# Kernel optimization log

Measured on AMD Instinct MI355X. Metric: run time of the kernel, lower is better.

## Reference

```python
import jax, jax.numpy as jnp
import numpy as np
import math

GROUPS = 32
EPS = 1e-5

def group_norm(x, w, b):
    B, C, H, W = x.shape
    xg = x.reshape(B, GROUPS, C // GROUPS, H, W)
    mu = xg.mean(axis=(2, 3, 4), keepdims=True)
    var = xg.var(axis=(2, 3, 4), keepdims=True)
    xn = ((xg - mu) * jax.lax.rsqrt(var + EPS)).reshape(B, C, H, W)
    return xn * w[None, :, None, None] + b[None, :, None, None]

def conv1x1(x, w, b):
    # x: [B,Cin,H,W], w: [Cout,Cin], b: [Cout]
    return jnp.einsum('bchw,oc->bohw', x, w) + b[None, :, None, None]

def setup_inputs() -> dict:
    key = jax.random.key(0)
    ks = jax.random.split(key, 8)
    B, C, E, H, W = 8, 256, 512, 64, 64
    x = jax.random.normal(ks[0], (B, C, H, W), dtype=jnp.float32)
    condA = jax.random.normal(ks[1], (B, E, H, W), dtype=jnp.float32)
    gn_x_w = jnp.ones((C,), jnp.float32)
    gn_x_b = jnp.zeros((C,), jnp.float32)
    gn_c_w = jnp.ones((E,), jnp.float32)
    gn_c_b = jnp.zeros((E,), jnp.float32)
    q_w = jax.random.normal(ks[2], (C, C), jnp.float32) * 0.02
    q_b = jnp.zeros((C,), jnp.float32)
    k_w = jax.random.normal(ks[3], (C, E), jnp.float32) * 0.02
    k_b = jnp.zeros((C,), jnp.float32)
    v_w = jax.random.normal(ks[4], (C, E), jnp.float32) * 0.02
    v_b = jnp.zeros((C,), jnp.float32)
    return {"x": x, "condA": condA, "gn_x_w": gn_x_w, "gn_x_b": gn_x_b,
            "gn_c_w": gn_c_w, "gn_c_b": gn_c_b, "q_w": q_w, "q_b": q_b,
            "k_w": k_w, "k_b": k_b, "v_w": v_w, "v_b": v_b}

def reference(x, condA, gn_x_w, gn_x_b, gn_c_w, gn_c_b, q_w, q_b, k_w, k_b, v_w, v_b):
    B, C, H, W = x.shape
    scale = math.sqrt(C)
    h = group_norm(x, gn_x_w, gn_x_b)
    h1 = group_norm(condA, gn_c_w, gn_c_b)
    q = conv1x1(h, q_w, q_b)      # [B,C,H,W]
    k = conv1x1(h1, k_w, k_b)     # [B,C,Hc,Wc]
    v = conv1x1(h1, v_w, v_b)     # [B,C,Hc,Wc]
    qf = q.transpose(0, 2, 3, 1).reshape(B, H * W, C)        # [B,N,C]
    kf = k.reshape(B, C, -1)                                  # [B,C,M]
    vf = v.transpose(0, 2, 3, 1).reshape(B, -1, C)            # [B,M,C]
    attn = jax.nn.softmax(jnp.einsum('bnc,bcm->bnm', qf, kf) / scale, axis=-1)
    out = jnp.einsum('bnm,bmc->bnc', attn, vf)                # [B,N,C]
    return out.reshape(B, H, W, C).transpose(0, 3, 1, 2)
```

## Files before the change

### kernel.cpp

```cpp
#include <hip/hip_runtime.h>


typedef _Float16 half8 __attribute__((ext_vector_type(8)));
typedef _Float16 half4v __attribute__((ext_vector_type(4)));
typedef float f32x4 __attribute__((ext_vector_type(4)));
typedef float f32x16 __attribute__((ext_vector_type(16)));

#define MFMA16(a, b, c) __builtin_amdgcn_mfma_f32_16x16x32_f16((a), (b), (c), 0, 0, 0)
#define MFMA32(a, b, c) __builtin_amdgcn_mfma_f32_32x32x16_f16((a), (b), (c), 0, 0, 0)

__global__ __launch_bounds__(256) void stats_kernel(
    const float* __restrict__ x, const float* __restrict__ condA,
    float* __restrict__ sx, float* __restrict__ sc) {
  int id = blockIdx.x;
  const float4* src;
  int nf4;
  float* dst;
  float inv_n;
  if (id < 256) {
    src = (const float4*)(x + (size_t)id * 32768);
    nf4 = 8192;
    dst = sx + id * 2;
    inv_n = 1.0f / 32768.0f;
  } else {
    int j = id - 256;
    src = (const float4*)(condA + (size_t)j * 65536);
    nf4 = 16384;
    dst = sc + j * 2;
    inv_n = 1.0f / 65536.0f;
  }
  int t = threadIdx.x;
  float s = 0.f, s2 = 0.f;
  for (int i = t; i < nf4; i += 256) {
    float4 v = src[i];
    s += v.x + v.y + v.z + v.w;
    s2 += v.x * v.x + v.y * v.y + v.z * v.z + v.w * v.w;
  }
#pragma unroll
  for (int m = 1; m <= 32; m <<= 1) {
    s += __shfl_xor(s, m, 64);
    s2 += __shfl_xor(s2, m, 64);
  }
  __shared__ float red[8];
  int w = t >> 6;
  if ((t & 63) == 0) { red[w * 2] = s; red[w * 2 + 1] = s2; }
  __syncthreads();
  if (t == 0) {
    float S = red[0] + red[2] + red[4] + red[6];
    float S2 = red[1] + red[3] + red[5] + red[7];
    float mu = S * inv_n;
    float var = S2 * inv_n - mu * mu;
    dst[0] = mu;
    dst[1] = rsqrtf(var + 1e-5f);
  }
}

template <int CH, int GS>
__global__ __launch_bounds__(256) void ntrans_kernel(
    const float* __restrict__ src, const float* __restrict__ stats,
    const float* __restrict__ gw, const float* __restrict__ gb,
    _Float16* __restrict__ dst) {
  int bid = blockIdx.x;
  int b = bid & 7, nt = (bid >> 3) & 63, ctile = bid >> 9;
  int n0 = nt * 64, c0 = ctile * 64;
  int t = threadIdx.x;
  __shared__ float tile[64][65];

  int cl = t >> 2;
  int c = c0 + cl;
  const float* st = stats + ((size_t)b * 32 + (c / GS)) * 2;
  float mu = st[0], rs = st[1];
  float a = rs * gw[c];
  float bb = gb[c] - mu * a;
  const float* srow = src + ((size_t)(b * CH + c)) * 4096 + n0 + (t & 3) * 16;
#pragma unroll
  for (int i = 0; i < 4; i++) {
    float4 v = *(const float4*)(srow + 4 * i);
    int nn = (t & 3) * 16 + 4 * i;
    tile[cl][nn + 0] = v.x * a + bb;
    tile[cl][nn + 1] = v.y * a + bb;
    tile[cl][nn + 2] = v.z * a + bb;
    tile[cl][nn + 3] = v.w * a + bb;
  }
  __syncthreads();
  int nl = t >> 2;
  half8 ov[2];
#pragma unroll
  for (int u = 0; u < 2; u++)
#pragma unroll
    for (int i = 0; i < 8; i++) ov[u][i] = (_Float16)tile[(t & 3) * 16 + 8 * u + i][nl];
  int n = n0 + nl;
  size_t tb = ((size_t)b * 256 + (n >> 4)) * (CH / 32);
  int ca = c0 + (t & 3) * 16;
#pragma unroll
  for (int u = 0; u < 2; u++) {
    int cc = ca + 8 * u;
    size_t addr = ((tb + (cc >> 5)) * 64 + (n & 15) + 16 * ((cc >> 3) & 3)) * 8;
    *(half8*)(dst + addr) = ov[u];
  }
}

__global__ __launch_bounds__(256) void wconv_kernel(
    const float* __restrict__ wq, const float* __restrict__ wk,
    const float* __restrict__ wv, _Float16* __restrict__ wqt,
    _Float16* __restrict__ wkt, _Float16* __restrict__ wvt) {
  int i = blockIdx.x * 256 + threadIdx.x;
  const float* src;
  _Float16* dst;
  int cin, ksbits, gi;
  if (i < 8192) { src = wq; dst = wqt; cin = 256; ksbits = 3; gi = i; }
  else if (i < 24576) { src = wk; dst = wkt; cin = 512; ksbits = 4; gi = i - 8192; }
  else if (i < 40960) { src = wv; dst = wvt; cin = 512; ksbits = 4; gi = i - 24576; }
  else return;
  int tile = gi >> 6, g = gi & 63;
  int otile = tile >> ksbits, ks = tile & ((1 << ksbits) - 1);
  int o = otile * 16 + (g & 15), k = ks * 32 + (g >> 4) * 8;
  const float* s = src + (size_t)o * cin + k;
  half8 hv;
#pragma unroll
  for (int j = 0; j < 8; j++) hv[j] = (_Float16)s[j];
  *(half8*)(dst + (size_t)gi * 8) = hv;
}

template <int CIN, int SCALE>
__global__ __launch_bounds__(256, 2) void projQK_kernel(
    const _Float16* __restrict__ Ht, const _Float16* __restrict__ Wt,
    const float* __restrict__ bias, _Float16* __restrict__ out) {
  int bid = blockIdx.x;
  int b = bid & 7, nt = (bid >> 3) & 31, ot = bid >> 8;
  int n0 = nt * 128, o0 = ot * 64;
  int t = threadIdx.x, l = t & 63, w = t >> 6;
  int c15 = l & 15, q = l >> 4;
  constexpr int KS = CIN / 32;

  const half8* ap = (const half8*)Wt + ((size_t)(ot * 4 + w) * KS) * 64 + l;
  const half8* bp = (const half8*)Ht + ((size_t)(b * 256 + nt * 8) * KS) * 64 + l;

  f32x4 acc[8] = {};
#pragma unroll
  for (int ks = 0; ks < KS; ks++) {
    half8 af = ap[ks * 64];
#pragma unroll
    for (int ct = 0; ct < 8; ct++)
      acc[ct] = MFMA16(af, bp[(ct * KS + ks) * 64], acc[ct]);
  }
  int o4 = o0 + w * 16 + 4 * q;
  f32x4 bv = *(const f32x4*)(bias + o4);
#pragma unroll
  for (int ct = 0; ct < 8; ct++) {
    int n = n0 + ct * 16 + c15;
    half4v hv;
#pragma unroll
    for (int r = 0; r < 4; r++) {
      float v = acc[ct][r] + bv[r];
      if (SCALE) v *= 0.0625f;
      hv[r] = (_Float16)v;
    }
    *(half4v*)(out + ((size_t)b * 4096 + n) * 256 + o4) = hv;
  }
}

__global__ __launch_bounds__(256, 2) void projV_kernel(
    const _Float16* __restrict__ Ht, const _Float16* __restrict__ Wt,
    const float* __restrict__ bias, _Float16* __restrict__ Vt) {
  int bid = blockIdx.x;
  int b = bid & 7, mt = (bid >> 3) & 63, ct2 = bid >> 9;
  int m0 = mt * 64, c0 = ct2 * 128;
  int t = threadIdx.x, l = t & 63, w = t >> 6;
  int c15 = l & 15, q = l >> 4;
  constexpr int KS = 16;

  const half8* ap = (const half8*)Ht + ((size_t)(b * 256 + mt * 4 + w) * KS) * 64 + l;
  const half8* bp = (const half8*)Wt + ((size_t)(c0 >> 4) * KS) * 64 + l;

  f32x4 acc[8] = {};
#pragma unroll
  for (int ks = 0; ks < KS; ks++) {
    half8 af = ap[ks * 64];
#pragma unroll
    for (int ct = 0; ct < 8; ct++)
      acc[ct] = MFMA16(af, bp[(ct * KS + ks) * 64], acc[ct]);
  }
  int m = m0 + w * 16 + 4 * q;
  size_t mbase = ((size_t)b * 256 + (m >> 4)) * 8;
#pragma unroll
  for (int ct = 0; ct < 8; ct++) {
    int c = c0 + ct * 16 + c15;
    float bs = bias[c];
    half4v pv4;
#pragma unroll
    for (int r = 0; r < 4; r++) pv4[r] = (_Float16)(acc[ct][r] + bs);
    size_t addr = ((mbase + (c >> 5)) * 64 + (c & 31) + ((q >> 1) << 5)) * 8 + (q & 1) * 4;
    *(half4v*)(Vt + addr) = pv4;
  }
}

__global__ __launch_bounds__(256, 2) void attn_kernel(
    const _Float16* __restrict__ Q, const _Float16* __restrict__ K,
    const _Float16* __restrict__ Vt, float* __restrict__ out) {
  int bid = blockIdx.x;
  int b = bid & 7, nt = bid >> 3;
  int n0 = nt * 64;
  int t = threadIdx.x, l = t & 63, w = t >> 6;
  int l31 = l & 31, h = l >> 5;
  int mh = w & 1, nh = w >> 1;

  __shared__ __align__(16) _Float16 kbuf[16384];
  __shared__ __align__(16) _Float16 pbuf[4096];
  __shared__ float lsw[2][64];

  half8 qf[16];
  {
    const _Float16* qb = Q + ((size_t)(b * 4096 + n0 + nh * 32 + l31)) * 256 + h * 8;
#pragma unroll
    for (int ks = 0; ks < 16; ks++) qf[ks] = *(const half8*)(qb + ks * 16);
  }

  const half8* kgl = (const half8*)(K + ((size_t)b * 4096 + w * 16 + h) * 256) + l31;
  int kwa[8];
  {
    int kblk = l31 >> 1, hw = l & 1;
    int swz = (kblk & 3) << 1;
    int mblk = w >> 1;
#pragma unroll
    for (int i = 0; i < 8; i++) {
      int m5 = ((w & 1) << 4) + 2 * i + h;
      int g = ((m5 ^ hw) | (hw << 5)) ^ swz;
      kwa[i] = (mblk * 16 + kblk) * 512 + g * 8;
    }
  }
  int gbase = (l31 ^ h) | (h << 5);

  const half8* vt8 = (const half8*)Vt + (size_t)b * 256 * 8 * 64;

  f32x16 acc_o[4] = {};
  float l_part = 0.f;

  half8 kreg[8];
#pragma unroll
  for (int i = 0; i < 8; i++) kreg[i] = kgl[i * 64];
#pragma unroll
  for (int i = 0; i < 8; i++) *(half8*)&kbuf[kwa[i]] = kreg[i];
  __syncthreads();

  for (int it = 0; it < 64; it++) {
    int itn = it < 63 ? it + 1 : 63;
#pragma unroll
    for (int i = 0; i < 8; i++) kreg[i] = kgl[itn * 2048 + i * 64];
    half8 vf0[8];
#pragma unroll
    for (int u = 0; u < 2; u++)
#pragma unroll
      for (int ct = 0; ct < 4; ct++)
        vf0[u * 4 + ct] = vt8[((size_t)(it * 4 + u) * 8 + (mh * 4 + ct)) * 64 + l];

    f32x16 s = {};
#pragma unroll
    for (int ks = 0; ks < 16; ks++) {
      half8 kf = *(const half8*)&kbuf[(mh * 16 + ks) * 512 + (gbase ^ ((ks & 3) << 1)) * 8];
      s = MFMA32(kf, qf[ks], s);
    }

    half4v pv[4];
#pragma unroll
    for (int k2 = 0; k2 < 4; k2++) {
#pragma unroll
      for (int r = 0; r < 4; r++) {
        float e = __expf(s[4 * k2 + r]);
        l_part += e;
        pv[k2][r] = (_Float16)e;
      }
    }
    __syncthreads();

#pragma unroll
    for (int k2 = 0; k2 < 4; k2++) {
      int hm = k2 & 1;
      int tau = nh * 4 + mh * 2 + (k2 >> 1);
      int g = (l31 ^ hm) | (hm << 5);
      *(half4v*)&pbuf[tau * 512 + g * 8 + 4 * h] = pv[k2];
    }
#pragma unroll
    for (int i = 0; i < 8; i++) *(half8*)&kbuf[kwa[i]] = kreg[i];
    __syncthreads();

    half8 vf1[8];
#pragma unroll
    for (int u = 0; u < 2; u++)
#pragma unroll
      for (int ct = 0; ct < 4; ct++)
        vf1[u * 4 + ct] = vt8[((size_t)(it * 4 + 2 + u) * 8 + (mh * 4 + ct)) * 64 + l];
#pragma unroll
    for (int ks = 0; ks < 2; ks++) {
      half8 pf = *(const half8*)&pbuf[(nh * 4 + ks) * 512 + gbase * 8];
#pragma unroll
      for (int ct = 0; ct < 4; ct++) acc_o[ct] = MFMA32(pf, vf0[ks * 4 + ct], acc_o[ct]);
    }
#pragma unroll
    for (int ks = 2; ks < 4; ks++) {
      half8 pf = *(const half8*)&pbuf[(nh * 4 + ks) * 512 + gbase * 8];
#pragma unroll
      for (int ct = 0; ct < 4; ct++) acc_o[ct] = MFMA32(pf, vf1[(ks - 2) * 4 + ct], acc_o[ct]);
    }
  }

  {
    float v = l_part + __shfl_xor(l_part, 32, 64);
    if (l < 32) lsw[mh][nh * 32 + l] = v;
  }
  __syncthreads();
#pragma unroll
  for (int k2 = 0; k2 < 4; k2++) {
    int nb = nh * 32 + 4 * h + 8 * k2;
    f32x4 s0 = *(const f32x4*)&lsw[0][nb];
    f32x4 s1 = *(const f32x4*)&lsw[1][nb];
    f32x4 linv;
#pragma unroll
    for (int r = 0; r < 4; r++) linv[r] = 1.0f / (s0[r] + s1[r]);
#pragma unroll
    for (int ct = 0; ct < 4; ct++) {
      int c = mh * 128 + ct * 32 + l31;
      f32x4 o4;
#pragma unroll
      for (int r = 0; r < 4; r++) o4[r] = acc_o[ct][4 * k2 + r] * linv[r];
      *(f32x4*)(out + ((size_t)(b * 256 + c)) * 4096 + n0 + nb) = o4;
    }
  }
}

extern "C" void kernel_launch(void* const* d_in, const int* in_sizes, int n_in,
                              void* d_out, int out_size, void* d_ws,
                              size_t ws_size, hipStream_t stream) {
  const float* x = (const float*)d_in[0];
  const float* condA = (const float*)d_in[1];
  const float* gxw = (const float*)d_in[2];
  const float* gxb = (const float*)d_in[3];
  const float* gcw = (const float*)d_in[4];
  const float* gcb = (const float*)d_in[5];
  const float* qw = (const float*)d_in[6];
  const float* qb = (const float*)d_in[7];
  const float* kw = (const float*)d_in[8];
  const float* kb = (const float*)d_in[9];
  const float* vw = (const float*)d_in[10];
  const float* vb = (const float*)d_in[11];
  float* out = (float*)d_out;

  char* ws = (char*)d_ws;
  float* statsx = (float*)(ws);
  float* statsc = (float*)(ws + 2048);
  _Float16* wqt = (_Float16*)(ws + 4096);
  _Float16* wkt = (_Float16*)(ws + 135168);
  _Float16* wvt = (_Float16*)(ws + 397312);
  char* p = ws + 659456;
  _Float16* hxTt = (_Float16*)p; p += (size_t)8 * 4096 * 256 * 2;
  _Float16* h1Tt = (_Float16*)p; p += (size_t)8 * 4096 * 512 * 2;
  _Float16* Qh = (_Float16*)p;   p += (size_t)8 * 4096 * 256 * 2;
  _Float16* Kh = (_Float16*)p;   p += (size_t)8 * 4096 * 256 * 2;
  _Float16* Vt = (_Float16*)p;

  stats_kernel<<<512, 256, 0, stream>>>(x, condA, statsx, statsc);
  ntrans_kernel<256, 8><<<2048, 256, 0, stream>>>(x, statsx, gxw, gxb, hxTt);
  ntrans_kernel<512, 16><<<4096, 256, 0, stream>>>(condA, statsc, gcw, gcb, h1Tt);
  wconv_kernel<<<160, 256, 0, stream>>>(qw, kw, vw, wqt, wkt, wvt);
  projQK_kernel<256, 1><<<1024, 256, 0, stream>>>(hxTt, wqt, qb, Qh);
  projQK_kernel<512, 0><<<1024, 256, 0, stream>>>(h1Tt, wkt, kb, Kh);
  projV_kernel<<<1024, 256, 0, stream>>>(h1Tt, wvt, vb, Vt);
  attn_kernel<<<512, 256, 0, stream>>>(Qh, Kh, Vt, out);
}
```

Baseline: 441.2 us.

## Merge prep kernels, fuse K/V projections with shared LDS tile, pre-tile Q/K for attention

```diff
diff --git a/kernel.cpp b/kernel.cpp
--- a/kernel.cpp
+++ b/kernel.cpp
@@ -9,27 +9,48 @@
 #define MFMA16(a, b, c) __builtin_amdgcn_mfma_f32_16x16x32_f16((a), (b), (c), 0, 0, 0)
 #define MFMA32(a, b, c) __builtin_amdgcn_mfma_f32_32x32x16_f16((a), (b), (c), 0, 0, 0)
 
-__global__ __launch_bounds__(256) void stats_kernel(
+__global__ __launch_bounds__(256) void statswconv_kernel(
     const float* __restrict__ x, const float* __restrict__ condA,
-    float* __restrict__ sx, float* __restrict__ sc) {
-  int id = blockIdx.x;
+    float* __restrict__ sx, float* __restrict__ sc,
+    const float* __restrict__ wq, const float* __restrict__ wk,
+    const float* __restrict__ wv, _Float16* __restrict__ wqt,
+    _Float16* __restrict__ wkt, _Float16* __restrict__ wvt) {
+  int bid = blockIdx.x;
+  int t = threadIdx.x;
+  if (bid >= 512) {
+    int i = (bid - 512) * 256 + t;
+    const float* src;
+    _Float16* dst;
+    int cin, ksbits, gi;
+    if (i < 8192) { src = wq; dst = wqt; cin = 256; ksbits = 3; gi = i; }
+    else if (i < 24576) { src = wk; dst = wkt; cin = 512; ksbits = 4; gi = i - 8192; }
+    else { src = wv; dst = wvt; cin = 512; ksbits = 4; gi = i - 24576; }
+    int tile = gi >> 6, g = gi & 63;
+    int otile = tile >> ksbits, ks = tile & ((1 << ksbits) - 1);
+    int o = otile * 16 + (g & 15), k = ks * 32 + (g >> 4) * 8;
+    const float* s = src + (size_t)o * cin + k;
+    half8 hv;
+#pragma unroll
+    for (int j = 0; j < 8; j++) hv[j] = (_Float16)s[j];
+    *(half8*)(dst + (size_t)gi * 8) = hv;
+    return;
+  }
   const float4* src;
   int nf4;
   float* dst;
   float inv_n;
-  if (id < 256) {
-    src = (const float4*)(x + (size_t)id * 32768);
+  if (bid < 256) {
+    src = (const float4*)(x + (size_t)bid * 32768);
     nf4 = 8192;
-    dst = sx + id * 2;
+    dst = sx + bid * 2;
     inv_n = 1.0f / 32768.0f;
   } else {
-    int j = id - 256;
+    int j = bid - 256;
     src = (const float4*)(condA + (size_t)j * 65536);
     nf4 = 16384;
     dst = sc + j * 2;
     inv_n = 1.0f / 65536.0f;
   }
-  int t = threadIdx.x;
   float s = 0.f, s2 = 0.f;
   for (int i = t; i < nf4; i += 256) {
     float4 v = src[i];
@@ -55,20 +76,31 @@
   }
 }
 
-template <int CH, int GS>
 __global__ __launch_bounds__(256) void ntrans_kernel(
-    const float* __restrict__ src, const float* __restrict__ stats,
-    const float* __restrict__ gw, const float* __restrict__ gb,
-    _Float16* __restrict__ dst) {
+    const float* __restrict__ x, const float* __restrict__ condA,
+    const float* __restrict__ statsx, const float* __restrict__ statsc,
+    const float* __restrict__ gxw, const float* __restrict__ gxb,
+    const float* __restrict__ gcw, const float* __restrict__ gcb,
+    _Float16* __restrict__ hxTt, _Float16* __restrict__ h1Tt) {
   int bid = blockIdx.x;
-  int b = bid & 7, nt = (bid >> 3) & 63, ctile = bid >> 9;
+  const float *src, *stats, *gw, *gb;
+  _Float16* dst;
+  int CH, gsh, bid2;
+  if (bid < 2048) {
+    src = x; stats = statsx; gw = gxw; gb = gxb; dst = hxTt;
+    CH = 256; gsh = 3; bid2 = bid;
+  } else {
+    src = condA; stats = statsc; gw = gcw; gb = gcb; dst = h1Tt;
+    CH = 512; gsh = 4; bid2 = bid - 2048;
+  }
+  int b = bid2 & 7, nt = (bid2 >> 3) & 63, ctile = bid2 >> 9;
   int n0 = nt * 64, c0 = ctile * 64;
   int t = threadIdx.x;
   __shared__ float tile[64][65];
 
   int cl = t >> 2;
   int c = c0 + cl;
-  const float* st = stats + ((size_t)b * 32 + (c / GS)) * 2;
+  const float* st = stats + ((size_t)b * 32 + (c >> gsh)) * 2;
   float mu = st[0], rs = st[1];
   float a = rs * gw[c];
   float bb = gb[c] - mu * a;
@@ -90,7 +122,7 @@
 #pragma unroll
     for (int i = 0; i < 8; i++) ov[u][i] = (_Float16)tile[(t & 3) * 16 + 8 * u + i][nl];
   int n = n0 + nl;
-  size_t tb = ((size_t)b * 256 + (n >> 4)) * (CH / 32);
+  size_t tb = ((size_t)b * 256 + (n >> 4)) * (CH >> 5);
   int ca = c0 + (t & 3) * 16;
 #pragma unroll
   for (int u = 0; u < 2; u++) {
@@ -100,103 +132,132 @@
   }
 }
 
-__global__ __launch_bounds__(256) void wconv_kernel(
-    const float* __restrict__ wq, const float* __restrict__ wk,
-    const float* __restrict__ wv, _Float16* __restrict__ wqt,
-    _Float16* __restrict__ wkt, _Float16* __restrict__ wvt) {
-  int i = blockIdx.x * 256 + threadIdx.x;
-  const float* src;
-  _Float16* dst;
-  int cin, ksbits, gi;
-  if (i < 8192) { src = wq; dst = wqt; cin = 256; ksbits = 3; gi = i; }
-  else if (i < 24576) { src = wk; dst = wkt; cin = 512; ksbits = 4; gi = i - 8192; }
-  else if (i < 40960) { src = wv; dst = wvt; cin = 512; ksbits = 4; gi = i - 24576; }
-  else return;
-  int tile = gi >> 6, g = gi & 63;
-  int otile = tile >> ksbits, ks = tile & ((1 << ksbits) - 1);
-  int o = otile * 16 + (g & 15), k = ks * 32 + (g >> 4) * 8;
-  const float* s = src + (size_t)o * cin + k;
-  half8 hv;
-#pragma unroll
-  for (int j = 0; j < 8; j++) hv[j] = (_Float16)s[j];
-  *(half8*)(dst + (size_t)gi * 8) = hv;
-}
-
-template <int CIN, int SCALE>
-__global__ __launch_bounds__(256, 2) void projQK_kernel(
+__global__ __launch_bounds__(256, 2) void projQ_kernel(
     const _Float16* __restrict__ Ht, const _Float16* __restrict__ Wt,
-    const float* __restrict__ bias, _Float16* __restrict__ out) {
+    const float* __restrict__ bias, _Float16* __restrict__ Qt) {
   int bid = blockIdx.x;
-  int b = bid & 7, nt = (bid >> 3) & 31, ot = bid >> 8;
-  int n0 = nt * 128, o0 = ot * 64;
+  int b = bid & 7, nt = bid >> 3;
   int t = threadIdx.x, l = t & 63, w = t >> 6;
   int c15 = l & 15, q = l >> 4;
-  constexpr int KS = CIN / 32;
-
-  const half8* ap = (const half8*)Wt + ((size_t)(ot * 4 + w) * KS) * 64 + l;
-  const half8* bp = (const half8*)Ht + ((size_t)(b * 256 + nt * 8) * KS) * 64 + l;
-
-  f32x4 acc[8] = {};
-#pragma unroll
-  for (int ks = 0; ks < KS; ks++) {
-    half8 af = ap[ks * 64];
-#pragma unroll
-    for (int ct = 0; ct < 8; ct++)
-      acc[ct] = MFMA16(af, bp[(ct * KS + ks) * 64], acc[ct]);
-  }
-  int o4 = o0 + w * 16 + 4 * q;
-  f32x4 bv = *(const f32x4*)(bias + o4);
-#pragma unroll
-  for (int ct = 0; ct < 8; ct++) {
-    int n = n0 + ct * 16 + c15;
-    half4v hv;
-#pragma unroll
-    for (int r = 0; r < 4; r++) {
-      float v = acc[ct][r] + bv[r];
-      if (SCALE) v *= 0.0625f;
-      hv[r] = (_Float16)v;
-    }
-    *(half4v*)(out + ((size_t)b * 4096 + n) * 256 + o4) = hv;
-  }
-}
-
-__global__ __launch_bounds__(256, 2) void projV_kernel(
-    const _Float16* __restrict__ Ht, const _Float16* __restrict__ Wt,
-    const float* __restrict__ bias, _Float16* __restrict__ Vt) {
+
+  __shared__ __align__(16) _Float16 hbuf[16384];
+  half8* hb = (half8*)hbuf;
+  {
+    const half8* sg = (const half8*)Ht + (size_t)(b * 256 + nt * 4) * 512;
+#pragma unroll
+    for (int i = 0; i < 8; i++) hb[t + 256 * i] = sg[t + 256 * i];
+  }
+  __syncthreads();
+
+  const half8* wt8 = (const half8*)Wt;
+#pragma unroll
+  for (int p = 0; p < 2; p++) {
+    int oa = (p * 4 + w) * 2;
+    f32x4 acc[2][4] = {};
+#pragma unroll
+    for (int ks = 0; ks < 8; ks++) {
+      half8 af0 = wt8[((size_t)(oa + 0) * 8 + ks) * 64 + l];
+      half8 af1 = wt8[((size_t)(oa + 1) * 8 + ks) * 64 + l];
+#pragma unroll
+      for (int nt2 = 0; nt2 < 4; nt2++) {
+        half8 bf = hb[(nt2 * 8 + ks) * 64 + l];
+        acc[0][nt2] = MFMA16(af0, bf, acc[0][nt2]);
+        acc[1][nt2] = MFMA16(af1, bf, acc[1][nt2]);
+      }
+    }
+#pragma unroll
+    for (int j = 0; j < 2; j++) {
+      int o4 = (oa + j) * 16 + 4 * q;
+      f32x4 bv = *(const f32x4*)(bias + o4);
+#pragma unroll
+      for (int nt2 = 0; nt2 < 4; nt2++) {
+        half4v hv;
+#pragma unroll
+        for (int r = 0; r < 4; r++) hv[r] = (_Float16)((acc[j][nt2][r] + bv[r]) * 0.0625f);
+        size_t addr = ((((size_t)b * 128 + nt * 2 + (nt2 >> 1)) * 16 + (oa + j)) * 64 +
+                       (nt2 & 1) * 16 + c15 + 32 * (q >> 1)) * 8 + (q & 1) * 4;
+        *(half4v*)(Qt + addr) = hv;
+      }
+    }
+  }
+}
+
+__global__ __launch_bounds__(256, 2) void projKV_kernel(
+    const _Float16* __restrict__ Ht, const _Float16* __restrict__ Wk,
+    const _Float16* __restrict__ Wv, const float* __restrict__ kb,
+    const float* __restrict__ vb, _Float16* __restrict__ Kt,
+    _Float16* __restrict__ Vt) {
   int bid = blockIdx.x;
-  int b = bid & 7, mt = (bid >> 3) & 63, ct2 = bid >> 9;
-  int m0 = mt * 64, c0 = ct2 * 128;
+  int b = bid & 7, mt = bid >> 3;
+  int m0 = mt * 64;
   int t = threadIdx.x, l = t & 63, w = t >> 6;
   int c15 = l & 15, q = l >> 4;
-  constexpr int KS = 16;
-
-  const half8* ap = (const half8*)Ht + ((size_t)(b * 256 + mt * 4 + w) * KS) * 64 + l;
-  const half8* bp = (const half8*)Wt + ((size_t)(c0 >> 4) * KS) * 64 + l;
-
-  f32x4 acc[8] = {};
-#pragma unroll
-  for (int ks = 0; ks < KS; ks++) {
-    half8 af = ap[ks * 64];
-#pragma unroll
-    for (int ct = 0; ct < 8; ct++)
-      acc[ct] = MFMA16(af, bp[(ct * KS + ks) * 64], acc[ct]);
-  }
-  int m = m0 + w * 16 + 4 * q;
-  size_t mbase = ((size_t)b * 256 + (m >> 4)) * 8;
-#pragma unroll
-  for (int ct = 0; ct < 8; ct++) {
-    int c = c0 + ct * 16 + c15;
-    float bs = bias[c];
-    half4v pv4;
-#pragma unroll
-    for (int r = 0; r < 4; r++) pv4[r] = (_Float16)(acc[ct][r] + bs);
-    size_t addr = ((mbase + (c >> 5)) * 64 + (c & 31) + ((q >> 1) << 5)) * 8 + (q & 1) * 4;
-    *(half4v*)(Vt + addr) = pv4;
+
+  __shared__ __align__(16) _Float16 hbuf[32768];
+  half8* hb = (half8*)hbuf;
+  {
+    const half8* sg = (const half8*)Ht + (size_t)(b * 256 + mt * 4) * 1024;
+#pragma unroll
+    for (int i = 0; i < 16; i++) hb[t + 256 * i] = sg[t + 256 * i];
+  }
+  __syncthreads();
+
+  const half8* wk8 = (const half8*)Wk;
+  const half8* wv8 = (const half8*)Wv;
+#pragma unroll
+  for (int p = 0; p < 2; p++) {
+    int oa = (p * 4 + w) * 2;
+    f32x4 acck[2][4] = {};
+    f32x4 accv[4][2] = {};
+#pragma unroll
+    for (int ks = 0; ks < 16; ks++) {
+      half8 kf0 = wk8[((size_t)(oa + 0) * 16 + ks) * 64 + l];
+      half8 kf1 = wk8[((size_t)(oa + 1) * 16 + ks) * 64 + l];
+      half8 vf0 = wv8[((size_t)(oa + 0) * 16 + ks) * 64 + l];
+      half8 vf1 = wv8[((size_t)(oa + 1) * 16 + ks) * 64 + l];
+#pragma unroll
+      for (int nt2 = 0; nt2 < 4; nt2++) {
+        half8 lf = hb[(nt2 * 16 + ks) * 64 + l];
+        acck[0][nt2] = MFMA16(kf0, lf, acck[0][nt2]);
+        acck[1][nt2] = MFMA16(kf1, lf, acck[1][nt2]);
+        accv[nt2][0] = MFMA16(lf, vf0, accv[nt2][0]);
+        accv[nt2][1] = MFMA16(lf, vf1, accv[nt2][1]);
+      }
+    }
+#pragma unroll
+    for (int j = 0; j < 2; j++) {
+      int o4 = (oa + j) * 16 + 4 * q;
+      f32x4 bv = *(const f32x4*)(kb + o4);
+#pragma unroll
+      for (int nt2 = 0; nt2 < 4; nt2++) {
+        half4v hv;
+#pragma unroll
+        for (int r = 0; r < 4; r++) hv[r] = (_Float16)(acck[j][nt2][r] + bv[r]);
+        size_t addr = ((((size_t)b * 128 + mt * 2 + (nt2 >> 1)) * 16 + (oa + j)) * 64 +
+                       (nt2 & 1) * 16 + c15 + 32 * (q >> 1)) * 8 + (q & 1) * 4;
+        *(half4v*)(Kt + addr) = hv;
+      }
+    }
+#pragma unroll
+    for (int nt2 = 0; nt2 < 4; nt2++) {
+      int m = m0 + nt2 * 16 + 4 * q;
+      size_t mbase = ((size_t)b * 256 + (m >> 4)) * 8;
+#pragma unroll
+      for (int j = 0; j < 2; j++) {
+        int c = (oa + j) * 16 + c15;
+        float bs = vb[c];
+        half4v hv;
+#pragma unroll
+        for (int r = 0; r < 4; r++) hv[r] = (_Float16)(accv[nt2][j][r] + bs);
+        size_t addr = ((mbase + (c >> 5)) * 64 + (c & 31) + ((q >> 1) << 5)) * 8 + (q & 1) * 4;
+        *(half4v*)(Vt + addr) = hv;
+      }
+    }
   }
 }
 
 __global__ __launch_bounds__(256, 2) void attn_kernel(
-    const _Float16* __restrict__ Q, const _Float16* __restrict__ K,
+    const _Float16* __restrict__ Qt, const _Float16* __restrict__ Kt,
     const _Float16* __restrict__ Vt, float* __restrict__ out) {
   int bid = blockIdx.x;
   int b = bid & 7, nt = bid >> 3;
@@ -208,45 +269,33 @@
   __shared__ __align__(16) _Float16 kbuf[16384];
   __shared__ __align__(16) _Float16 pbuf[4096];
   __shared__ float lsw[2][64];
+  half8* kb8 = (half8*)kbuf;
 
   half8 qf[16];
   {
-    const _Float16* qb = Q + ((size_t)(b * 4096 + n0 + nh * 32 + l31)) * 256 + h * 8;
-#pragma unroll
-    for (int ks = 0; ks < 16; ks++) qf[ks] = *(const half8*)(qb + ks * 16);
-  }
-
-  const half8* kgl = (const half8*)(K + ((size_t)b * 4096 + w * 16 + h) * 256) + l31;
-  int kwa[8];
-  {
-    int kblk = l31 >> 1, hw = l & 1;
-    int swz = (kblk & 3) << 1;
-    int mblk = w >> 1;
-#pragma unroll
-    for (int i = 0; i < 8; i++) {
-      int m5 = ((w & 1) << 4) + 2 * i + h;
-      int g = ((m5 ^ hw) | (hw << 5)) ^ swz;
-      kwa[i] = (mblk * 16 + kblk) * 512 + g * 8;
-    }
-  }
-  int gbase = (l31 ^ h) | (h << 5);
-
+    const half8* qt8 = (const half8*)Qt + ((size_t)(b * 128 + nt * 2 + nh) * 16) * 64 + l;
+#pragma unroll
+    for (int ks = 0; ks < 16; ks++) qf[ks] = qt8[ks * 64];
+  }
+
+  const half8* ktb = (const half8*)Kt + (size_t)b * 131072 + t;
   const half8* vt8 = (const half8*)Vt + (size_t)b * 256 * 8 * 64;
+  int gb = (l31 ^ h) | (h << 5);
 
   f32x16 acc_o[4] = {};
   float l_part = 0.f;
 
   half8 kreg[8];
 #pragma unroll
-  for (int i = 0; i < 8; i++) kreg[i] = kgl[i * 64];
-#pragma unroll
-  for (int i = 0; i < 8; i++) *(half8*)&kbuf[kwa[i]] = kreg[i];
+  for (int i = 0; i < 8; i++) kreg[i] = ktb[256 * i];
+#pragma unroll
+  for (int i = 0; i < 8; i++) kb8[t + 256 * i] = kreg[i];
   __syncthreads();
 
   for (int it = 0; it < 64; it++) {
     int itn = it < 63 ? it + 1 : 63;
 #pragma unroll
-    for (int i = 0; i < 8; i++) kreg[i] = kgl[itn * 2048 + i * 64];
+    for (int i = 0; i < 8; i++) kreg[i] = ktb[itn * 2048 + 256 * i];
     half8 vf0[8];
 #pragma unroll
     for (int u = 0; u < 2; u++)
@@ -257,7 +306,7 @@
     f32x16 s = {};
 #pragma unroll
     for (int ks = 0; ks < 16; ks++) {
-      half8 kf = *(const half8*)&kbuf[(mh * 16 + ks) * 512 + (gbase ^ ((ks & 3) << 1)) * 8];
+      half8 kf = kb8[(mh * 16 + ks) * 64 + l];
       s = MFMA32(kf, qf[ks], s);
     }
 
@@ -281,7 +330,7 @@
       *(half4v*)&pbuf[tau * 512 + g * 8 + 4 * h] = pv[k2];
     }
 #pragma unroll
-    for (int i = 0; i < 8; i++) *(half8*)&kbuf[kwa[i]] = kreg[i];
+    for (int i = 0; i < 8; i++) kb8[t + 256 * i] = kreg[i];
     __syncthreads();
 
     half8 vf1[8];
@@ -292,13 +341,13 @@
         vf1[u * 4 + ct] = vt8[((size_t)(it * 4 + 2 + u) * 8 + (mh * 4 + ct)) * 64 + l];
 #pragma unroll
     for (int ks = 0; ks < 2; ks++) {
-      half8 pf = *(const half8*)&pbuf[(nh * 4 + ks) * 512 + gbase * 8];
+      half8 pf = *(const half8*)&pbuf[(nh * 4 + ks) * 512 + gb * 8];
 #pragma unroll
       for (int ct = 0; ct < 4; ct++) acc_o[ct] = MFMA32(pf, vf0[ks * 4 + ct], acc_o[ct]);
     }
 #pragma unroll
     for (int ks = 2; ks < 4; ks++) {
-      half8 pf = *(const half8*)&pbuf[(nh * 4 + ks) * 512 + gbase * 8];
+      half8 pf = *(const half8*)&pbuf[(nh * 4 + ks) * 512 + gb * 8];
 #pragma unroll
       for (int ct = 0; ct < 4; ct++) acc_o[ct] = MFMA32(pf, vf1[(ks - 2) * 4 + ct], acc_o[ct]);
     }
@@ -354,16 +403,15 @@
   char* p = ws + 659456;
   _Float16* hxTt = (_Float16*)p; p += (size_t)8 * 4096 * 256 * 2;
   _Float16* h1Tt = (_Float16*)p; p += (size_t)8 * 4096 * 512 * 2;
-  _Float16* Qh = (_Float16*)p;   p += (size_t)8 * 4096 * 256 * 2;
-  _Float16* Kh = (_Float16*)p;   p += (size_t)8 * 4096 * 256 * 2;
+  _Float16* Qt = (_Float16*)p;   p += (size_t)8 * 4096 * 256 * 2;
+  _Float16* Kt = (_Float16*)p;   p += (size_t)8 * 4096 * 256 * 2;
   _Float16* Vt = (_Float16*)p;
 
-  stats_kernel<<<512, 256, 0, stream>>>(x, condA, statsx, statsc);
-  ntrans_kernel<256, 8><<<2048, 256, 0, stream>>>(x, statsx, gxw, gxb, hxTt);
-  ntrans_kernel<512, 16><<<4096, 256, 0, stream>>>(condA, statsc, gcw, gcb, h1Tt);
-  wconv_kernel<<<160, 256, 0, stream>>>(qw, kw, vw, wqt, wkt, wvt);
-  projQK_kernel<256, 1><<<1024, 256, 0, stream>>>(hxTt, wqt, qb, Qh);
-  projQK_kernel<512, 0><<<1024, 256, 0, stream>>>(h1Tt, wkt, kb, Kh);
-  projV_kernel<<<1024, 256, 0, stream>>>(h1Tt, wvt, vb, Vt);
-  attn_kernel<<<512, 256, 0, stream>>>(Qh, Kh, Vt, out);
-}
+  statswconv_kernel<<<672, 256, 0, stream>>>(x, condA, statsx, statsc,
+                                             qw, kw, vw, wqt, wkt, wvt);
+  ntrans_kernel<<<6144, 256, 0, stream>>>(x, condA, statsx, statsc,
+                                          gxw, gxb, gcw, gcb, hxTt, h1Tt);
+  projQ_kernel<<<512, 256, 0, stream>>>(hxTt, wqt, qb, Qt);
+  projKV_kernel<<<512, 256, 0, stream>>>(h1Tt, wkt, wvt, kb, vb, Kt, Vt);
+  attn_kernel<<<512, 256, 0, stream>>>(Qt, Kt, Vt, out);
+}
```

Result: faster. 393.6 us (-10.8%).
